# Performance work log

Measured on AMD Instinct MI355X. Metric: run time of the kernel, lower is better.

Reference implementation:

```python
import jax, jax.numpy as jnp
import numpy as np

LAMBDA_SOFTMAX = 9.0  # SCAN temperature
LEAKY_SLOPE = 0.1
EPS = 1e-8


def l2norm(x, axis=-1):
    return x / (jnp.linalg.norm(x, axis=axis, keepdims=True) + EPS)


def cosine(a, b, axis=-1):
    num = jnp.sum(a * b, axis=axis)
    den = jnp.linalg.norm(a, axis=axis) * jnp.linalg.norm(b, axis=axis) + EPS
    return num / den


def setup_inputs() -> dict:
    key = jax.random.key(0)
    k1, k2, k3, k4 = jax.random.split(key, 4)
    B, L, R = 128, 512, 512
    Dt, Di, D = 300, 1024, 256
    text = jax.random.normal(k1, (B, L, Dt), dtype=jnp.float32)
    image = jax.random.normal(k2, (B, R, Di), dtype=jnp.float32)
    Wt = jax.random.normal(k3, (Dt, D), dtype=jnp.float32) * (1.0 / np.sqrt(Dt))
    Wi = jax.random.normal(k4, (Di, D), dtype=jnp.float32) * (1.0 / np.sqrt(Di))
    bt = jnp.zeros((D,), dtype=jnp.float32)
    bi = jnp.zeros((D,), dtype=jnp.float32)
    return {"text": text, "image": image, "Wt": Wt, "bt": bt, "Wi": Wi, "bi": bi}


def reference(text, image, Wt, bt, Wi, bi):
    # Feature extractors: linear projection + L2 normalization
    tf = l2norm(jnp.einsum('ble,ed->bld', text, Wt) + bt)    # (B, L, D) text word features
    imf = l2norm(jnp.einsum('bre,ed->brd', image, Wi) + bi)  # (B, R, D) image region features

    # Preassign attention: per-pair word/region similarity (shared by both directions)
    A = jnp.einsum('bld,brd->blr', tf, imf)                  # (B, L, R)
    A = jax.nn.leaky_relu(A, LEAKY_SLOPE)

    # Text-to-image: each word attends over image regions
    S_tti = jax.nn.softmax(LAMBDA_SOFTMAX * A, axis=-1)      # (B, L, R)
    image_ss = jnp.einsum('blr,brd->bld', S_tti, imf)        # (B, L, D) shared semantic per word
    image_ss_relevance = jnp.mean(cosine(tf, image_ss), axis=1)  # (B,)

    # Image-to-text: each region attends over text words
    S_itt = jax.nn.softmax(LAMBDA_SOFTMAX * A, axis=1)       # (B, L, R)
    text_ss = jnp.einsum('blr,bld->brd', S_itt, tf)          # (B, R, D) shared semantic per region
    text_ss_relevance = jnp.mean(cosine(text_ss, imf), axis=1)   # (B,)

    return image_ss_relevance + text_ss_relevance
```

## Files before the change

kernel.cpp:

```cpp
#include <hip/hip_runtime.h>
#include <math.h>

#define EPSV 1e-8f

constexpr int BB = 128;
constexpr int NROW = 512;
constexpr int DT = 300;
constexpr int DI = 1024;
constexpr int DD = 256;
constexpr int NB2 = (BB * NROW) / 64;

typedef __bf16 bf16x8 __attribute__((ext_vector_type(8)));
typedef float f32x4 __attribute__((ext_vector_type(4)));

__device__ inline unsigned short f2bf(float f) {
  unsigned int x = __builtin_bit_cast(unsigned int, f);
  unsigned int r = (x + 0x7fffu + ((x >> 16) & 1u)) >> 16;
  return (unsigned short)r;
}
__device__ inline float bf2f(unsigned short u) {
  return __builtin_bit_cast(float, (unsigned int)u << 16);
}

__global__ __launch_bounds__(256) void prep_w(
    const float* __restrict__ W, unsigned short* __restrict__ Wt, int E, int Ep) {
  __shared__ float tile[32][36];
  const int t = threadIdx.x;
  const int e0 = blockIdx.x * 32, n0 = blockIdx.y * 32;
  {
    const int r = t >> 3, c4 = (t & 7) * 4;
    float4 v = {0.f, 0.f, 0.f, 0.f};
    if (e0 + r < E) v = *reinterpret_cast<const float4*>(&W[(size_t)(e0 + r) * DD + n0 + c4]);
    tile[r][c4] = v.x; tile[r][c4 + 1] = v.y; tile[r][c4 + 2] = v.z; tile[r][c4 + 3] = v.w;
  }
  __syncthreads();
  {
    const int n = t >> 3, e4 = (t & 7) * 4;
    uint2 pk;
    pk.x = f2bf(tile[e4][n]) | ((unsigned)f2bf(tile[e4 + 1][n]) << 16);
    pk.y = f2bf(tile[e4 + 2][n]) | ((unsigned)f2bf(tile[e4 + 3][n]) << 16);
    *reinterpret_cast<uint2*>(&Wt[(size_t)(n0 + n) * Ep + e0 + e4]) = pk;
  }
}

__global__ __launch_bounds__(256, 3) void proj_mfma_fused(
    const float* __restrict__ Xi, const float* __restrict__ Xt,
    const unsigned short* __restrict__ Wti, const unsigned short* __restrict__ Wtt,
    const float* __restrict__ bi, const float* __restrict__ bt,
    unsigned short* __restrict__ Ybi, unsigned short* __restrict__ Yti,
    unsigned short* __restrict__ Ybt, unsigned short* __restrict__ Ytt) {
  __shared__ __align__(16) unsigned char smem[32768];
  unsigned short* Xs = (unsigned short*)smem;
  unsigned short* Ws = (unsigned short*)(smem + 5120);
  float* red2 = (float*)smem;
  unsigned short* rp = (unsigned short*)smem;

  const bool isImg = blockIdx.x < NB2;
  const float* X = isImg ? Xi : Xt;
  const unsigned short* Wt = isImg ? Wti : Wtt;
  const float* bias = isImg ? bi : bt;
  unsigned short* Yb = isImg ? Ybi : Ybt;
  unsigned short* Yt = isImg ? Yti : Ytt;
  const int E = isImg ? DI : DT;
  const int Ep = isImg ? 1024 : 320;
  const int row0 = (isImg ? blockIdx.x : blockIdx.x - NB2) * 64;

  const int t = threadIdx.x;
  const int l = t & 63, w = t >> 6;
  const int q15 = l & 15, h = l >> 4;

  f32x4 acc[4][4];
#pragma unroll
  for (int rt = 0; rt < 4; ++rt)
#pragma unroll
    for (int ct = 0; ct < 4; ++ct) acc[rt][ct] = (f32x4){0.f, 0.f, 0.f, 0.f};

  const int sxr = t >> 2, sxq = t & 3;

  for (int e0 = 0; e0 < Ep; e0 += 32) {
    __syncthreads();
    {
      const int eb = e0 + sxq * 8;
      float4 a = {0.f, 0.f, 0.f, 0.f}, b4 = {0.f, 0.f, 0.f, 0.f};
      const float* xp = &X[(size_t)(row0 + sxr) * E + eb];
      if (eb + 4 <= E) a = *reinterpret_cast<const float4*>(xp);
      if (eb + 8 <= E) b4 = *reinterpret_cast<const float4*>(xp + 4);
      uint4 u;
      u.x = f2bf(a.x) | ((unsigned)f2bf(a.y) << 16);
      u.y = f2bf(a.z) | ((unsigned)f2bf(a.w) << 16);
      u.z = f2bf(b4.x) | ((unsigned)f2bf(b4.y) << 16);
      u.w = f2bf(b4.z) | ((unsigned)f2bf(b4.w) << 16);
      *reinterpret_cast<uint4*>(&Xs[sxr * 40 + sxq * 8]) = u;
    }
    {
#pragma unroll
      for (int i = 0; i < 4; ++i) {
        const int c = t + i * 256;
        const int row = c >> 2, c8 = (c & 3) * 8;
        const uint4 u = *reinterpret_cast<const uint4*>(&Wt[(size_t)row * Ep + e0 + c8]);
        *reinterpret_cast<uint4*>(&Ws[row * 40 + c8]) = u;
      }
    }
    __syncthreads();
    bf16x8 af[4], bfr[4];
#pragma unroll
    for (int rt = 0; rt < 4; ++rt)
      af[rt] = *reinterpret_cast<const bf16x8*>(&Xs[(rt * 16 + q15) * 40 + h * 8]);
#pragma unroll
    for (int ct = 0; ct < 4; ++ct)
      bfr[ct] = *reinterpret_cast<const bf16x8*>(&Ws[(w * 64 + ct * 16 + q15) * 40 + h * 8]);
#pragma unroll
    for (int rt = 0; rt < 4; ++rt)
#pragma unroll
      for (int ct = 0; ct < 4; ++ct)
        acc[rt][ct] = __builtin_amdgcn_mfma_f32_16x16x32_bf16(af[rt], bfr[ct], acc[rt][ct], 0, 0, 0);
  }

  float bias_v[4];
#pragma unroll
  for (int ct = 0; ct < 4; ++ct) bias_v[ct] = bias[w * 64 + ct * 16 + q15];
#pragma unroll
  for (int rt = 0; rt < 4; ++rt)
#pragma unroll
    for (int ct = 0; ct < 4; ++ct)
#pragma unroll
      for (int r = 0; r < 4; ++r) acc[rt][ct][r] += bias_v[ct];

  float ss[4][4];
#pragma unroll
  for (int rt = 0; rt < 4; ++rt)
#pragma unroll
    for (int r = 0; r < 4; ++r) {
      float s = 0.f;
#pragma unroll
      for (int ct = 0; ct < 4; ++ct) s = fmaf(acc[rt][ct][r], acc[rt][ct][r], s);
      s += __shfl_xor(s, 1, 64);
      s += __shfl_xor(s, 2, 64);
      s += __shfl_xor(s, 4, 64);
      s += __shfl_xor(s, 8, 64);
      ss[rt][r] = s;
    }

  __syncthreads();
  if (q15 == 0) {
#pragma unroll
    for (int rt = 0; rt < 4; ++rt)
#pragma unroll
      for (int r = 0; r < 4; ++r)
        red2[(rt * 16 + h * 4 + r) * 4 + w] = ss[rt][r];
  }
  __syncthreads();
  float inv[4][4];
#pragma unroll
  for (int rt = 0; rt < 4; ++rt)
#pragma unroll
    for (int r = 0; r < 4; ++r) {
      const float4 p = *reinterpret_cast<const float4*>(&red2[(rt * 16 + h * 4 + r) * 4]);
      inv[rt][r] = 1.f / (sqrtf(p.x + p.y + p.z + p.w) + EPSV);
    }
  __syncthreads();

  const int bb = row0 >> 9;
  const int rin0 = row0 & 511;
#pragma unroll
  for (int rt = 0; rt < 4; ++rt) {
#pragma unroll
    for (int ct = 0; ct < 4; ++ct) {
      unsigned short uv[4];
#pragma unroll
      for (int r = 0; r < 4; ++r) uv[r] = f2bf(acc[rt][ct][r] * inv[rt][r]);
      const int col = w * 64 + ct * 16 + q15;
#pragma unroll
      for (int r = 0; r < 4; ++r)
        rp[(rt * 16 + h * 4 + r) * 256 + col] = uv[r];
      unsigned long long pk = (unsigned long long)uv[0] |
                              ((unsigned long long)uv[1] << 16) |
                              ((unsigned long long)uv[2] << 32) |
                              ((unsigned long long)uv[3] << 48);
      const int rin = rin0 + rt * 16 + h * 4;
      *reinterpret_cast<unsigned long long*>(&Yt[((size_t)bb * DD + col) * NROW + rin]) = pk;
    }
  }
  __syncthreads();
#pragma unroll
  for (int i = 0; i < 8; ++i) {
    const int s = t + i * 256;
    const int row = s >> 5, c = s & 31;
    const uint4 v = *reinterpret_cast<const uint4*>(&rp[row * 256 + c * 8]);
    *reinterpret_cast<uint4*>(&Yb[(size_t)(row0 + row) * DD + c * 8]) = v;
  }
}

__global__ __launch_bounds__(512, 4) void cross_attn_fused(
    const unsigned short* __restrict__ tf,
    const unsigned short* __restrict__ imf,
    const unsigned short* __restrict__ tft,
    const unsigned short* __restrict__ imft,
    float* __restrict__ out, float invN) {
  __shared__ __align__(16) unsigned short K_lds[32 * 264];
  __shared__ __align__(16) unsigned short Vt_lds[256 * 40];
  __shared__ __align__(16) unsigned short P_lds[8][16 * 40];

  const int dir = blockIdx.z;
  const unsigned short* Qg  = dir ? imf : tf;
  const unsigned short* Kg  = dir ? tf : imf;
  const unsigned short* Vtg = dir ? tft : imft;

  const int t = threadIdx.x;
  const int l = t & 63;
  const int w = t >> 6;
  const int h = l >> 4;
  const int q15 = l & 15;
  const int b = blockIdx.x;
  const int qbase = blockIdx.y * 128 + w * 16;
  const size_t qrow0 = (size_t)b * NROW + qbase;
  const size_t kband = (size_t)b * NROW * DD;
  const size_t vband = (size_t)b * DD * NROW;

  bf16x8 qf[8];
#pragma unroll
  for (int kc = 0; kc < 8; ++kc)
    qf[kc] = *reinterpret_cast<const bf16x8*>(
        &Qg[(qrow0 + q15) * DD + kc * 32 + h * 8]);

  f32x4 accO[16];
#pragma unroll
  for (int nt = 0; nt < 16; ++nt) accO[nt] = (f32x4){0.f, 0.f, 0.f, 0.f};
  float denom = 0.f;
  float dotq = 0.f;

  for (int c0 = 0; c0 < NROW; c0 += 32) {
    __syncthreads();
#pragma unroll
    for (int i = 0; i < 2; ++i) {
      const int slot = t + i * 512;
      const int row = slot >> 5, cc = slot & 31;
      const uint4 v = *reinterpret_cast<const uint4*>(
          &Kg[kband + (size_t)(c0 + row) * DD + cc * 8]);
      *reinterpret_cast<uint4*>(&K_lds[row * 264 + cc * 8]) = v;
    }
#pragma unroll
    for (int i = 0; i < 2; ++i) {
      const int slot = t + i * 512;
      const int d = slot >> 2, cc = slot & 3;
      const uint4 v = *reinterpret_cast<const uint4*>(
          &Vtg[vband + (size_t)d * NROW + c0 + cc * 8]);
      *reinterpret_cast<uint4*>(&Vt_lds[d * 40 + cc * 8]) = v;
    }
    __syncthreads();

    f32x4 accS[2];
#pragma unroll
    for (int kvt = 0; kvt < 2; ++kvt) accS[kvt] = (f32x4){0.f, 0.f, 0.f, 0.f};
#pragma unroll
    for (int kc = 0; kc < 8; ++kc) {
#pragma unroll
      for (int kvt = 0; kvt < 2; ++kvt) {
        const bf16x8 kf = *reinterpret_cast<const bf16x8*>(
            &K_lds[(kvt * 16 + q15) * 264 + kc * 32 + h * 8]);
        accS[kvt] = __builtin_amdgcn_mfma_f32_16x16x32_bf16(
            kf, qf[kc], accS[kvt], 0, 0, 0);
      }
    }

#pragma unroll
    for (int kvt = 0; kvt < 2; ++kvt) {
      float p[4];
#pragma unroll
      for (int r = 0; r < 4; ++r) {
        const float s = accS[kvt][r];
        const float a = (s > 0.f) ? s : 0.1f * s;
        p[r] = __expf(9.f * a - 9.f);
        denom += p[r];
        dotq = fmaf(p[r], s, dotq);
      }
      uint2 pk;
      pk.x = f2bf(p[0]) | ((unsigned)f2bf(p[1]) << 16);
      pk.y = f2bf(p[2]) | ((unsigned)f2bf(p[3]) << 16);
      *reinterpret_cast<uint2*>(
          &P_lds[w][q15 * 40 + kvt * 16 + h * 4]) = pk;
    }

    const bf16x8 pf = *reinterpret_cast<const bf16x8*>(
        &P_lds[w][q15 * 40 + h * 8]);
#pragma unroll
    for (int nt = 0; nt < 16; ++nt) {
      const bf16x8 vf = *reinterpret_cast<const bf16x8*>(
          &Vt_lds[(nt * 16 + q15) * 40 + h * 8]);
      accO[nt] = __builtin_amdgcn_mfma_f32_16x16x32_bf16(
          pf, vf, accO[nt], 0, 0, 0);
    }
  }

  denom += __shfl_xor(denom, 16, 64);
  denom += __shfl_xor(denom, 32, 64);
  dotq += __shfl_xor(dotq, 16, 64);
  dotq += __shfl_xor(dotq, 32, 64);
  float total = 0.f;
#pragma unroll
  for (int r = 0; r < 4; ++r) {
    float o2 = 0.f;
#pragma unroll
    for (int nt = 0; nt < 16; ++nt) {
      const float ov = accO[nt][r];
      o2 = fmaf(ov, ov, o2);
    }
#pragma unroll
    for (int off = 1; off < 16; off <<= 1) o2 += __shfl_xor(o2, off, 64);
    const int qrow = h * 4 + r;
    const float dnq = __shfl(denom, qrow, 64);
    const float dq  = __shfl(dotq, qrow, 64);
    total += dq / (sqrtf(o2) + dnq * EPSV);
  }
  total += __shfl_xor(total, 16, 64);
  total += __shfl_xor(total, 32, 64);
  if (l == 0) atomicAdd(&out[b], invN * total);
}

extern "C" void kernel_launch(void* const* d_in, const int* in_sizes, int n_in,
                              void* d_out, int out_size, void* d_ws, size_t ws_size,
                              hipStream_t stream) {
  const float* text  = (const float*)d_in[0];
  const float* image = (const float*)d_in[1];
  const float* Wt    = (const float*)d_in[2];
  const float* bt    = (const float*)d_in[3];
  const float* Wi    = (const float*)d_in[4];
  const float* bi    = (const float*)d_in[5];
  float* out = (float*)d_out;

  constexpr size_t NE = (size_t)BB * NROW * DD;
  unsigned short* tf   = (unsigned short*)d_ws;
  unsigned short* imf  = tf + NE;
  unsigned short* tft  = imf + NE;
  unsigned short* imft = tft + NE;
  unsigned short* wtt  = imft + NE;
  unsigned short* wti  = wtt + (size_t)DD * 320;

  hipMemsetAsync(out, 0, sizeof(float) * BB, stream);

  prep_w<<<dim3(320 / 32, 8), 256, 0, stream>>>(Wt, wtt, DT, 320);
  prep_w<<<dim3(1024 / 32, 8), 256, 0, stream>>>(Wi, wti, DI, 1024);

  proj_mfma_fused<<<dim3(2 * NB2), 256, 0, stream>>>(
      image, text, wti, wtt, bi, bt, imf, imft, tf, tft);

  cross_attn_fused<<<dim3(BB, NROW / 128, 2), 512, 0, stream>>>(
      tf, imf, tft, imft, out, 1.0f / NROW);
}
```

Before: 294.8 us.

## Double-buffer projection GEMM with direct global-to-LDS weight loads and swizzle

The projection kernel now double-buffers its X and W tiles in shared memory. It prefetches the next K-slice while MFMAs run on the current one, which removes one barrier per iteration. Weight tiles go straight from global memory into LDS via global_load_lds. To keep LDS reads free of bank conflicts without padding, prep_w writes the transposed bf16 weights in an XOR-swizzled column order. Shared memory use grows to about 42KB, which may lower occupancy relative to the 3-blocks launch bound.

```diff
diff --git a/kernel.cpp b/kernel.cpp
--- a/kernel.cpp
+++ b/kernel.cpp
@@ -36,10 +36,12 @@
   __syncthreads();
   {
     const int n = t >> 3, e4 = (t & 7) * 4;
+    const int nrow = n0 + n;
+    const int e4p = e4 ^ ((nrow & 3) * 8);
     uint2 pk;
     pk.x = f2bf(tile[e4][n]) | ((unsigned)f2bf(tile[e4 + 1][n]) << 16);
     pk.y = f2bf(tile[e4 + 2][n]) | ((unsigned)f2bf(tile[e4 + 3][n]) << 16);
-    *reinterpret_cast<uint2*>(&Wt[(size_t)(n0 + n) * Ep + e0 + e4]) = pk;
+    *reinterpret_cast<uint2*>(&Wt[(size_t)nrow * Ep + e0 + e4p]) = pk;
   }
 }
 
@@ -49,11 +51,14 @@
     const float* __restrict__ bi, const float* __restrict__ bt,
     unsigned short* __restrict__ Ybi, unsigned short* __restrict__ Yti,
     unsigned short* __restrict__ Ybt, unsigned short* __restrict__ Ytt) {
-  __shared__ __align__(16) unsigned char smem[32768];
-  unsigned short* Xs = (unsigned short*)smem;
-  unsigned short* Ws = (unsigned short*)(smem + 5120);
-  float* red2 = (float*)smem;
-  unsigned short* rp = (unsigned short*)smem;
+  __shared__ union {
+    struct {
+      unsigned short Wb[2][256 * 32];
+      unsigned short Xb[2][64 * 40];
+    } s;
+    float red2[64 * 4];
+    unsigned short rp[64 * 256];
+  } sm;
 
   const bool isImg = blockIdx.x < NB2;
   const float* X = isImg ? Xi : Xt;
@@ -77,43 +82,64 @@
 
   const int sxr = t >> 2, sxq = t & 3;
 
+  float4 xa, xb;
+  auto loadX = [&](int e0) {
+    const int eb = e0 + sxq * 8;
+    xa = (float4){0.f, 0.f, 0.f, 0.f};
+    xb = (float4){0.f, 0.f, 0.f, 0.f};
+    const float* xp = &X[(size_t)(row0 + sxr) * E + eb];
+    if (eb + 4 <= E) xa = *reinterpret_cast<const float4*>(xp);
+    if (eb + 8 <= E) xb = *reinterpret_cast<const float4*>(xp + 4);
+  };
+  auto writeX = [&](int buf) {
+    uint4 u;
+    u.x = f2bf(xa.x) | ((unsigned)f2bf(xa.y) << 16);
+    u.y = f2bf(xa.z) | ((unsigned)f2bf(xa.w) << 16);
+    u.z = f2bf(xb.x) | ((unsigned)f2bf(xb.y) << 16);
+    u.w = f2bf(xb.z) | ((unsigned)f2bf(xb.w) << 16);
+    *reinterpret_cast<uint4*>(&sm.s.Xb[buf][sxr * 40 + sxq * 8]) = u;
+  };
+  auto stageW = [&](int e0, int buf) {
+#pragma unroll
+    for (int i = 0; i < 4; ++i) {
+      const int idx = i * 2048 + w * 512 + l * 8;
+      const int row = idx >> 5, col = idx & 31;
+      __builtin_amdgcn_global_load_lds(
+          (const void*)&Wt[(size_t)row * Ep + e0 + col],
+          (void*)&sm.s.Wb[buf][i * 2048 + w * 512], 16, 0, 0);
+    }
+  };
+
+  stageW(0, 0);
+  loadX(0);
+  writeX(0);
+  __syncthreads();
+
+  int cur = 0;
   for (int e0 = 0; e0 < Ep; e0 += 32) {
-    __syncthreads();
-    {
-      const int eb = e0 + sxq * 8;
-      float4 a = {0.f, 0.f, 0.f, 0.f}, b4 = {0.f, 0.f, 0.f, 0.f};
-      const float* xp = &X[(size_t)(row0 + sxr) * E + eb];
-      if (eb + 4 <= E) a = *reinterpret_cast<const float4*>(xp);
-      if (eb + 8 <= E) b4 = *reinterpret_cast<const float4*>(xp + 4);
-      uint4 u;
-      u.x = f2bf(a.x) | ((unsigned)f2bf(a.y) << 16);
-      u.y = f2bf(a.z) | ((unsigned)f2bf(a.w) << 16);
-      u.z = f2bf(b4.x) | ((unsigned)f2bf(b4.y) << 16);
-      u.w = f2bf(b4.z) | ((unsigned)f2bf(b4.w) << 16);
-      *reinterpret_cast<uint4*>(&Xs[sxr * 40 + sxq * 8]) = u;
-    }
-    {
-#pragma unroll
-      for (int i = 0; i < 4; ++i) {
-        const int c = t + i * 256;
-        const int row = c >> 2, c8 = (c & 3) * 8;
-        const uint4 u = *reinterpret_cast<const uint4*>(&Wt[(size_t)row * Ep + e0 + c8]);
-        *reinterpret_cast<uint4*>(&Ws[row * 40 + c8]) = u;
-      }
-    }
-    __syncthreads();
+    const int nxt = cur ^ 1;
+    const bool more = (e0 + 32) < Ep;
+    if (more) {
+      stageW(e0 + 32, nxt);
+      loadX(e0 + 32);
+    }
     bf16x8 af[4], bfr[4];
 #pragma unroll
     for (int rt = 0; rt < 4; ++rt)
-      af[rt] = *reinterpret_cast<const bf16x8*>(&Xs[(rt * 16 + q15) * 40 + h * 8]);
+      af[rt] = *reinterpret_cast<const bf16x8*>(
+          &sm.s.Xb[cur][(rt * 16 + q15) * 40 + h * 8]);
 #pragma unroll
     for (int ct = 0; ct < 4; ++ct)
-      bfr[ct] = *reinterpret_cast<const bf16x8*>(&Ws[(w * 64 + ct * 16 + q15) * 40 + h * 8]);
+      bfr[ct] = *reinterpret_cast<const bf16x8*>(
+          &sm.s.Wb[cur][(w * 64 + ct * 16 + q15) * 32 + ((h ^ (q15 & 3)) * 8)]);
 #pragma unroll
     for (int rt = 0; rt < 4; ++rt)
 #pragma unroll
       for (int ct = 0; ct < 4; ++ct)
         acc[rt][ct] = __builtin_amdgcn_mfma_f32_16x16x32_bf16(af[rt], bfr[ct], acc[rt][ct], 0, 0, 0);
+    if (more) writeX(nxt);
+    __syncthreads();
+    cur = nxt;
   }
 
   float bias_v[4];
@@ -147,7 +173,7 @@
     for (int rt = 0; rt < 4; ++rt)
 #pragma unroll
       for (int r = 0; r < 4; ++r)
-        red2[(rt * 16 + h * 4 + r) * 4 + w] = ss[rt][r];
+        sm.red2[(rt * 16 + h * 4 + r) * 4 + w] = ss[rt][r];
   }
   __syncthreads();
   float inv[4][4];
@@ -155,7 +181,7 @@
   for (int rt = 0; rt < 4; ++rt)
 #pragma unroll
     for (int r = 0; r < 4; ++r) {
-      const float4 p = *reinterpret_cast<const float4*>(&red2[(rt * 16 + h * 4 + r) * 4]);
+      const float4 p = *reinterpret_cast<const float4*>(&sm.red2[(rt * 16 + h * 4 + r) * 4]);
       inv[rt][r] = 1.f / (sqrtf(p.x + p.y + p.z + p.w) + EPSV);
     }
   __syncthreads();
@@ -172,7 +198,7 @@
       const int col = w * 64 + ct * 16 + q15;
 #pragma unroll
       for (int r = 0; r < 4; ++r)
-        rp[(rt * 16 + h * 4 + r) * 256 + col] = uv[r];
+        sm.rp[(rt * 16 + h * 4 + r) * 256 + col] = uv[r];
       unsigned long long pk = (unsigned long long)uv[0] |
                               ((unsigned long long)uv[1] << 16) |
                               ((unsigned long long)uv[2] << 32) |
@@ -186,7 +212,7 @@
   for (int i = 0; i < 8; ++i) {
     const int s = t + i * 256;
     const int row = s >> 5, c = s & 31;
-    const uint4 v = *reinterpret_cast<const uint4*>(&rp[row * 256 + c * 8]);
+    const uint4 v = *reinterpret_cast<const uint4*>(&sm.rp[row * 256 + c * 8]);
     *reinterpret_cast<uint4*>(&Yb[(size_t)(row0 + row) * DD + c * 8]) = v;
   }
 }
```

After: 326.7 us. 10.8% more time.
